# Kernel optimization log

Hardware: AMD Instinct MI355X
Metric: run time of the kernel (lower is better)

## Reference

```python
import jax, jax.numpy as jnp
import numpy as np

N = 100000
E = 1600000
D = 128          # in_feat == hidden_size
L = 3            # hidden layers
EPS = 1e-5       # BatchNorm1d eps


def setup_inputs() -> dict:
    key = jax.random.key(0)
    ks = jax.random.split(key, 12)
    x = jax.random.normal(ks[0], (N, D), dtype=jnp.float32)
    edge_index = jax.random.randint(ks[1], (2, E), 0, N, dtype=jnp.int64)
    s = 1.0 / np.sqrt(D)
    # stacked hidden-layer SAGEConv params: lin_l (neighbor), lin_r (root), bias on lin_l
    Wl = jax.random.uniform(ks[2], (L, D, D), jnp.float32, -s, s)
    Wr = jax.random.uniform(ks[3], (L, D, D), jnp.float32, -s, s)
    b = jax.random.uniform(ks[4], (L, D), jnp.float32, -s, s)
    # batchnorm affine params
    gamma = jnp.ones((L, D), jnp.float32)
    beta = jnp.zeros((L, D), jnp.float32)
    # output SAGEConv: D -> 1
    Wl_out = jax.random.uniform(ks[5], (D, 1), jnp.float32, -s, s)
    Wr_out = jax.random.uniform(ks[6], (D, 1), jnp.float32, -s, s)
    b_out = jax.random.uniform(ks[7], (1,), jnp.float32, -s, s)
    return {"x": x, "edge_index": edge_index, "Wl": Wl, "Wr": Wr, "b": b,
            "gamma": gamma, "beta": beta, "Wl_out": Wl_out, "Wr_out": Wr_out,
            "b_out": b_out}


def _sage(x, src, dst, inv_deg, Wl, Wr, b):
    # gather neighbor features along edges, mean-aggregate at destination
    msg_sum = jax.ops.segment_sum(x[src], dst, num_segments=N)   # [N, F]
    mean = msg_sum * inv_deg                                     # 0 for isolated nodes
    return mean @ Wl + x @ Wr + b


def _batchnorm(x, gamma, beta):
    m = jnp.mean(x, axis=0)
    v = jnp.mean((x - m) ** 2, axis=0)  # biased var, as torch BN uses for normalization
    return gamma * (x - m) * jax.lax.rsqrt(v + EPS) + beta


def reference(x, edge_index, Wl, Wr, b, gamma, beta, Wl_out, Wr_out, b_out):
    src, dst = edge_index[0], edge_index[1]
    deg = jax.ops.segment_sum(jnp.ones((E,), x.dtype), dst, num_segments=N)
    inv_deg = jnp.where(deg > 0, 1.0 / jnp.maximum(deg, 1.0), 0.0)[:, None]
    h = x
    for i in range(L):
        h = _sage(h, src, dst, inv_deg, Wl[i], Wr[i], b[i])
        h = jax.nn.relu(h)
        h = _batchnorm(h, gamma[i], beta[i])
    out = _sage(h, src, dst, inv_deg, Wl_out, Wr_out, b_out)
    return jax.nn.sigmoid(out)  # [N, 1]
```

## Files before the change

kernel.cpp:

```cpp
#include <hip/hip_runtime.h>

typedef unsigned short u16;
typedef unsigned int u32;
typedef unsigned long long u64;

#define GN 100000
#define GE 1600000
#define DCAP 64
#define NRANGE 196
#define NBKT (NRANGE * 8)
#define BCAP 1536

typedef __bf16 bf16x8 __attribute__((ext_vector_type(8)));
typedef float f32x4 __attribute__((ext_vector_type(4)));
typedef float f32x2 __attribute__((ext_vector_type(2)));
typedef u32 u32x4 __attribute__((ext_vector_type(4)));
typedef u32 u32x2 __attribute__((ext_vector_type(2)));

__device__ __forceinline__ float bl(u32 u){ return __uint_as_float(u << 16); }
__device__ __forceinline__ float bh(u32 u){ return __uint_as_float(u & 0xffff0000u); }
__device__ __forceinline__ float bfu(u16 v){ return __uint_as_float(((u32)v) << 16); }
__device__ __forceinline__ u16 f2bf(float f){
    u32 u = __float_as_uint(f);
    u32 r = (u + 0x7fffu + ((u >> 16) & 1u)) >> 16;
    return (u16)r;
}
__device__ __forceinline__ u32 pack2(float a, float b){
    return (u32)f2bf(a) | ((u32)f2bf(b) << 16);
}
__device__ __forceinline__ u32 pk8x4(float a, float b, float c, float d){
    u32 p = (u32)__builtin_amdgcn_cvt_pk_fp8_f32(a, b, 0, false);
    p = (u32)__builtin_amdgcn_cvt_pk_fp8_f32(c, d, p, true);
    return p;
}

__global__ void __launch_bounds__(256) k_init(const int* ei, const u32* xraw,
                                              int* cursor, float* colpart, int* flags,
                                              int* bcur, float* scshbuf){
    int i = blockIdx.x * 256 + threadIdx.x;
    if (i < GN) cursor[i] = 0;
    if (i < NBKT) bcur[i] = 0;
    if (i < 6144) colpart[i] = 0.f;
    if (i < 256) scshbuf[i] = (i < 128) ? 1.f : 0.f;
    int t = threadIdx.x;
    if (blockIdx.x == 0){
        __shared__ int s_any[4];
        int v = 0;
        #pragma unroll
        for (int j = 0; j < 4; ++j){
            int k = t * 4 + j;
            v |= ei[2 * k * 1000 + 1];
        }
        #pragma unroll
        for (int m = 1; m < 64; m <<= 1) v |= __shfl_xor(v, m);
        if ((t & 63) == 0) s_any[t >> 6] = v;
        __syncthreads();
        if (t == 0){
            int any = s_any[0] | s_any[1] | s_any[2] | s_any[3];
            flags[0] = (any == 0) ? 1 : 0;
        }
    }
    if (blockIdx.x == 1){
        __shared__ int s_cnt[4];
        int cnt = 0;
        #pragma unroll
        for (int j = 0; j < 4; ++j){
            int idx = (t * 4 + j) * 6000 + 3;
            u32 u = xraw[idx];
            int e = (u >> 7) & 0xFF;
            cnt += (e >= 100 && e <= 140) ? 1 : 0;
        }
        #pragma unroll
        for (int m = 1; m < 64; m <<= 1) cnt += __shfl_xor(cnt, m);
        if ((t & 63) == 0) s_cnt[t >> 6] = cnt;
        __syncthreads();
        if (t == 0){
            int tot = s_cnt[0] + s_cnt[1] + s_cnt[2] + s_cnt[3];
            flags[1] = (tot > 512) ? 0 : 1;
        }
    }
}

__global__ void __launch_bounds__(256) k_convx(const void* x, const int* flags,
                                               u16* xb, u32* h8){
    int gid = blockIdx.x * 256 + threadIdx.x;
    if (gid >= GN * 16) return;
    float f0,f1,f2,f3,f4,f5,f6,f7;
    if (flags[1]){
        const u32x4* xf = (const u32x4*)x;
        u32x4 a = __builtin_nontemporal_load(xf + gid * 2);
        u32x4 b = __builtin_nontemporal_load(xf + gid * 2 + 1);
        f0 = __uint_as_float(a.x); f1 = __uint_as_float(a.y);
        f2 = __uint_as_float(a.z); f3 = __uint_as_float(a.w);
        f4 = __uint_as_float(b.x); f5 = __uint_as_float(b.y);
        f6 = __uint_as_float(b.z); f7 = __uint_as_float(b.w);
    } else {
        u32x4 g = __builtin_nontemporal_load((const u32x4*)x + gid);
        f0 = bl(g.x); f1 = bh(g.x); f2 = bl(g.y); f3 = bh(g.y);
        f4 = bl(g.z); f5 = bh(g.z); f6 = bl(g.w); f7 = bh(g.w);
    }
    u32x4 o;
    o.x = pack2(f0, f1); o.y = pack2(f2, f3);
    o.z = pack2(f4, f5); o.w = pack2(f6, f7);
    ((u32x4*)xb)[gid] = o;
    u32x2 e = { pk8x4(f0, f1, f2, f3), pk8x4(f4, f5, f6, f7) };
    ((u32x2*)h8)[gid] = e;
}

__global__ void __launch_bounds__(256) k_tofp8(const u16* h, u32* h8){
    int gid = blockIdx.x * 256 + threadIdx.x;
    if (gid >= GN * 16) return;
    u32x4 g = ((const u32x4*)h)[gid];
    u32x2 e = { pk8x4(bl(g.x), bh(g.x), bl(g.y), bh(g.y)),
                pk8x4(bl(g.z), bh(g.z), bl(g.w), bh(g.w)) };
    ((u32x2*)h8)[gid] = e;
}

#define WOFF_WR    49152
#define WOFF_B     98304
#define WOFF_G     98688
#define WOFF_BE    99072
#define WOFF_WLO   99456
#define WOFF_WRO   99584
#define WOFF_BO    99712
#define WTOT       99713
__global__ void __launch_bounds__(256) k_convw(const void* Wl, const void* Wr, const void* b,
                                               const void* g, const void* be, const void* wlo,
                                               const void* wro, const void* bo,
                                               const int* flags, u16* wbuf, float* biasf){
    int i = blockIdx.x * 256 + threadIdx.x;
    if (i >= WTOT) return;
    const void* s; int k;
    if (i < WOFF_B){
        const void* src = (i < WOFF_WR) ? Wl : Wr;
        int r = (i < WOFF_WR) ? i : i - WOFF_WR;
        int layer = r >> 14, L = r & 16383;
        int kk = ((L >> 10) << 3) | (L & 7);
        int cc = (L >> 3) & 127;
        int si = layer * 16384 + kk * 128 + cc;
        float fv = flags[1] ? ((const float*)src)[si] : bfu(((const u16*)src)[si]);
        wbuf[i] = f2bf(fv);
        return;
    }
    if      (i < WOFF_G  ){ s = b;   k = i - WOFF_B; }
    else if (i < WOFF_BE ){ s = g;   k = i - WOFF_G; }
    else if (i < WOFF_WLO){ s = be;  k = i - WOFF_BE; }
    else if (i < WOFF_WRO){ s = wlo; k = i - WOFF_WLO; }
    else if (i < WOFF_BO ){ s = wro; k = i - WOFF_WRO; }
    else                  { s = bo;  k = 0; }
    float fv = flags[1] ? ((const float*)s)[k] : bfu(((const u16*)s)[k]);
    wbuf[i] = f2bf(fv);
    if (i >= WOFF_B && i < WOFF_B + 384) biasf[i - WOFF_B] = fv;
}

__global__ void __launch_bounds__(256) k_fillA(const int* ei, const int* flags,
                                               int* bcur, u64* pairs){
    __shared__ int cnt[256];
    __shared__ int lofs[256];
    __shared__ int gbase[NRANGE];
    __shared__ u64 lp[1024];
    int t = threadIdx.x;
    int res = blockIdx.x & 7;
    int base = blockIdx.x * 1024;
    int is64 = flags[0];
    cnt[t] = 0;
    __syncthreads();
    int myd[4], mys[4], slot[4], myr[4];
    #pragma unroll
    for (int j = 0; j < 4; ++j){
        int e = base + j * 256 + t;
        if (e < GE){
            int d, s;
            if (is64){ d = __builtin_nontemporal_load(ei + 2 * (GE + e));
                       s = __builtin_nontemporal_load(ei + 2 * e); }
            else     { d = __builtin_nontemporal_load(ei + GE + e);
                       s = __builtin_nontemporal_load(ei + e); }
            myd[j] = d; mys[j] = s; myr[j] = d >> 9;
            slot[j] = atomicAdd(&cnt[myr[j]], 1);
        } else myr[j] = -1;
    }
    __syncthreads();
    int v = cnt[t];
    lofs[t] = v; __syncthreads();
    for (int off = 1; off < 256; off <<= 1){
        int u = (t >= off) ? lofs[t - off] : 0;
        __syncthreads();
        lofs[t] += u;
        __syncthreads();
    }
    int incl = lofs[t];
    __syncthreads();
    lofs[t] = incl - v;
    __syncthreads();
    #pragma unroll
    for (int j = 0; j < 4; ++j){
        if (myr[j] >= 0)
            lp[lofs[myr[j]] + slot[j]] = ((u64)(u32)myd[j] << 32) | (u32)mys[j];
    }
    if (t < NRANGE && cnt[t] > 0)
        gbase[t] = atomicAdd(&bcur[t * 8 + res], cnt[t]);
    __syncthreads();
    int total = GE - base; if (total > 1024) total = 1024;
    for (int i = t; i < total; i += 256){
        u64 pr = lp[i];
        int r = (int)(pr >> 32) >> 9;
        int g = gbase[r] + (i - lofs[r]);
        if (g < BCAP) pairs[((size_t)(r * 8 + res)) * BCAP + g] = pr;
    }
}

__global__ void __launch_bounds__(256) k_fillB(const int* bcur, const u64* pairs,
                                               int* cursor, int* col){
    int range = blockIdx.x % 200;
    int sub   = blockIdx.x / 200;
    if (range >= NRANGE || sub >= 8) return;
    int bkt = range * 8 + sub;
    int n = bcur[bkt]; if (n > BCAP) n = BCAP;
    const u64* P = pairs + (size_t)bkt * BCAP;
    for (int i = threadIdx.x; i < n; i += 256){
        u64 pr = __builtin_nontemporal_load(P + i);
        int s = (int)(u32)pr, d = (int)(pr >> 32);
        int pos = atomicAdd(&cursor[d], 1);
        if (pos < DCAP) col[d * DCAP + pos] = s;
    }
}

__global__ void __launch_bounds__(64) k_agg(const u32* h8, const int* deg, const int* col,
                                            u16* amean){
    int lane = threadIdx.x;
    int grp = lane >> 4;
    int lg  = lane & 15;
    int node = blockIdx.x * 4 + grp;
    if (node >= GN) return;
    int d = deg[node];
    int cnt = d < DCAP ? d : DCAP;
    const int* nb = col + node * DCAP;
    const u32x2* hrow = (const u32x2*)h8;
    float a0=0.f,a1=0.f,a2=0.f,a3=0.f,a4=0.f,a5=0.f,a6=0.f,a7=0.f;
    int e = 0;
    #define ACC8(v) { \
        f32x2 d0 = __builtin_amdgcn_cvt_pk_f32_fp8((v).x, false); \
        f32x2 d1 = __builtin_amdgcn_cvt_pk_f32_fp8((v).x, true);  \
        f32x2 d2 = __builtin_amdgcn_cvt_pk_f32_fp8((v).y, false); \
        f32x2 d3 = __builtin_amdgcn_cvt_pk_f32_fp8((v).y, true);  \
        a0 += d0.x; a1 += d0.y; a2 += d1.x; a3 += d1.y;           \
        a4 += d2.x; a5 += d2.y; a6 += d3.x; a7 += d3.y; }
    for (; e + 7 < cnt; e += 8){
        u32x2 v0 = hrow[(size_t)nb[e]     * 16 + lg];
        u32x2 v1 = hrow[(size_t)nb[e + 1] * 16 + lg];
        u32x2 v2 = hrow[(size_t)nb[e + 2] * 16 + lg];
        u32x2 v3 = hrow[(size_t)nb[e + 3] * 16 + lg];
        u32x2 v4 = hrow[(size_t)nb[e + 4] * 16 + lg];
        u32x2 v5 = hrow[(size_t)nb[e + 5] * 16 + lg];
        u32x2 v6 = hrow[(size_t)nb[e + 6] * 16 + lg];
        u32x2 v7 = hrow[(size_t)nb[e + 7] * 16 + lg];
        ACC8(v0) ACC8(v1) ACC8(v2) ACC8(v3) ACC8(v4) ACC8(v5) ACC8(v6) ACC8(v7)
    }
    for (; e + 1 < cnt; e += 2){
        u32x2 v0 = hrow[(size_t)nb[e]     * 16 + lg];
        u32x2 v1 = hrow[(size_t)nb[e + 1] * 16 + lg];
        ACC8(v0) ACC8(v1)
    }
    if (e < cnt){
        u32x2 v0 = hrow[(size_t)nb[e] * 16 + lg];
        ACC8(v0)
    }
    #undef ACC8
    float inv = (d > 0) ? 1.f / (float)d : 0.f;
    u32x4 o;
    o.x = pack2(a0 * inv, a1 * inv);
    o.y = pack2(a2 * inv, a3 * inv);
    o.z = pack2(a4 * inv, a5 * inv);
    o.w = pack2(a6 * inv, a7 * inv);
    ((u32x4*)amean)[(size_t)node * 16 + lg] = o;
}

__global__ void __launch_bounds__(256, 4) k_gemm(const u16* amean, const u16* hin,
                                                 const u16* Wl, const u16* Wr,
                                                 const float* biasf, const float* scsh,
                                                 u16* hout, float* colpart){
    __shared__ __align__(16) u16 wlds[16384];
    int t = threadIdx.x;
    int wid = t >> 6, lane = t & 63;
    int quad = lane >> 4, l15 = lane & 15;
    int r0 = blockIdx.x * 128 + wid * 32;
    int rowa = r0 + l15, rowb = rowa + 16;
    f32x4 acc[2][8];
    #pragma unroll
    for (int i = 0; i < 2; i++)
        #pragma unroll
        for (int j = 0; j < 8; j++) acc[i][j] = (f32x4){0.f, 0.f, 0.f, 0.f};

    #pragma unroll
    for (int half = 0; half < 2; ++half){
        const u16* W = half ? Wr : Wl;
        const u16* A = half ? hin : amean;
        if (half) __syncthreads();
        for (int j = t; j < 2048; j += 256){
            u32x4 g = ((const u32x4*)W)[j];
            int k0 = (j >> 7) << 3;
            f32x4 s0 = *(const f32x4*)(scsh + k0);
            f32x4 s1 = *(const f32x4*)(scsh + k0 + 4);
            u32x4 o;
            o.x = pack2(bl(g.x) * s0.x, bh(g.x) * s0.y);
            o.y = pack2(bl(g.y) * s0.z, bh(g.y) * s0.w);
            o.z = pack2(bl(g.z) * s1.x, bh(g.z) * s1.y);
            o.w = pack2(bl(g.w) * s1.z, bh(g.w) * s1.w);
            ((u32x4*)wlds)[j] = o;
        }
        __syncthreads();
        #pragma unroll
        for (int s = 0; s < 4; ++s){
            int kk = (s << 5) + (quad << 3);
            union { u32x4 u; bf16x8 v; } fa0, fa1;
            fa0.u = (rowa < GN) ? *(const u32x4*)(A + rowa * 128 + kk) : (u32x4){0,0,0,0};
            fa1.u = (rowb < GN) ? *(const u32x4*)(A + rowb * 128 + kk) : (u32x4){0,0,0,0};
            int kc = (s << 2) + quad;
            const u16* wb = &wlds[(kc << 10) + (l15 << 3)];
            #pragma unroll
            for (int cb = 0; cb < 8; ++cb){
                union { u32x4 u; bf16x8 v; } fb;
                fb.u = *(const u32x4*)(wb + (cb << 7));
                acc[0][cb] = __builtin_amdgcn_mfma_f32_16x16x32_bf16(fa0.v, fb.v, acc[0][cb], 0, 0, 0);
                acc[1][cb] = __builtin_amdgcn_mfma_f32_16x16x32_bf16(fa1.v, fb.v, acc[1][cb], 0, 0, 0);
            }
        }
    }
    __syncthreads();
    float* sst = (float*)wlds;
    sst[t] = 0.f;
    __syncthreads();

    float bsv[8];
    #pragma unroll
    for (int cb = 0; cb < 8; cb++) bsv[cb] = biasf[cb * 16 + l15];

    #pragma unroll
    for (int cb = 0; cb < 8; cb++){
        float csum = 0.f, csq = 0.f;
        #pragma unroll
        for (int rb = 0; rb < 2; rb++){
            int rbase = r0 + rb * 16 + quad * 4;
            #pragma unroll
            for (int rr = 0; rr < 4; rr++){
                int row = rbase + rr;
                float v = acc[rb][cb][rr] + bsv[cb];
                v = fmaxf(v, 0.f);
                if (row < GN) hout[row * 128 + cb * 16 + l15] = f2bf(v);
                float vm = (row < GN) ? v : 0.f;
                csum += vm; csq += vm * vm;
            }
        }
        csum += __shfl_xor(csum, 16); csum += __shfl_xor(csum, 32);
        csq  += __shfl_xor(csq, 16);  csq  += __shfl_xor(csq, 32);
        if (quad == 0){
            atomicAdd(&sst[cb * 16 + l15], csum);
            atomicAdd(&sst[128 + cb * 16 + l15], csq);
        }
    }
    __syncthreads();
    atomicAdd(&colpart[(blockIdx.x & 7) * 256 + t], sst[t]);
}

__global__ void __launch_bounds__(256) k_bnf(const float* colpart, const u16* gamma, const u16* beta,
                                             float* scshout, int mode,
                                             const u16* WlN, const u16* WrN,
                                             const float* bNsrc, float* bNdst,
                                             const u16* wlo, const u16* wro, const u16* bo,
                                             u16* hwl, u16* hwr, float* hb){
    __shared__ float s_sc[128], s_sh[128], s_red[256];
    int t = threadIdx.x;
    if (t < 128){
        float s = 0.f, q = 0.f;
        #pragma unroll
        for (int j = 0; j < 8; ++j){
            s += colpart[j * 256 + t];
            q += colpart[j * 256 + 128 + t];
        }
        const float invn = 1.f / (float)GN;
        float mean = s * invn;
        float var = fmaxf(q * invn - mean * mean, 0.f);
        float rstd = rsqrtf(var + 1e-5f);
        float g  = bfu(gamma[t]);
        float be = bfu(beta[t]);
        float sc = g * rstd, sh = be - mean * sc;
        scshout[t] = sc; scshout[128 + t] = sh;
        s_sc[t] = sc; s_sh[t] = sh;
    }
    __syncthreads();
    if (mode == 0){
        if (t < 128){
            float acc = bNsrc[t];
            for (int k = 0; k < 128; ++k){
                int L = ((k >> 3) << 10) + (t << 3) + (k & 7);
                acc += s_sh[k] * (bfu(WlN[L]) + bfu(WrN[L]));
            }
            bNdst[t] = acc;
        }
    } else {
        float contrib = 0.f;
        if (t < 128){
            float wl = bfu(wlo[t]), wr = bfu(wro[t]);
            hwl[t] = f2bf(s_sc[t] * wl);
            hwr[t] = f2bf(s_sc[t] * wr);
            contrib = s_sh[t] * (wl + wr);
        }
        s_red[t] = contrib;
        __syncthreads();
        for (int off = 128; off >= 1; off >>= 1){
            if (t < off) s_red[t] += s_red[t + off];
            __syncthreads();
        }
        if (t == 0) hb[0] = s_red[0] + bfu(bo[0]);
    }
}

__global__ void __launch_bounds__(256) k_dot(const u16* h, const u16* wl, const u16* wr,
                                             float* y, float* r){
    int node = (blockIdx.x * 256 + threadIdx.x) >> 6;
    int lane = threadIdx.x & 63;
    if (node >= GN) return;
    u32 hv  = ((const u32*)h)[node * 64 + lane];
    u32 wlv = ((const u32*)wl)[lane];
    u32 wrv = ((const u32*)wr)[lane];
    float hlo = bl(hv), hhi = bh(hv);
    float ya = hlo * bl(wlv) + hhi * bh(wlv);
    float ra = hlo * bl(wrv) + hhi * bh(wrv);
    #pragma unroll
    for (int m = 1; m < 64; m <<= 1){ ya += __shfl_xor(ya, m); ra += __shfl_xor(ra, m); }
    if (lane == 0){ y[node] = ya; r[node] = ra; }
}

__global__ void __launch_bounds__(256) k_out(const float* y, const float* r, const int* deg,
                                             const int* col, const float* hb,
                                             const int* flags, void* out){
    int n = blockIdx.x * 256 + threadIdx.x;
    if (n >= GN) return;
    int d = deg[n];
    int cnt = d < DCAP ? d : DCAP;
    const int* nb = col + n * DCAP;
    float s = 0.f;
    for (int e = 0; e < cnt; ++e) s += y[nb[e]];
    float inv = (d > 0) ? 1.f / (float)d : 0.f;
    float z = inv * s + r[n] + hb[0];
    float sg = 1.f / (1.f + __expf(-z));
    if (flags[1]) ((float*)out)[n] = sg;
    else          ((u16*)out)[n] = f2bf(sg);
}

extern "C" void kernel_launch(void* const* d_in, const int* in_sizes, int n_in,
                              void* d_out, int out_size, void* d_ws, size_t ws_size,
                              hipStream_t stream) {
    const void* x     = d_in[0];
    const int*  ei    = (const int*)d_in[1];
    const void* Wl    = d_in[2];
    const void* Wr    = d_in[3];
    const void* bias  = d_in[4];
    const void* gamma = d_in[5];
    const void* beta  = d_in[6];
    const void* wlout = d_in[7];
    const void* wrout = d_in[8];
    const void* bout  = d_in[9];

    char* p = (char*)d_ws;
    auto take = [&](size_t b){ void* q = (void*)p; p += (b + 255) & ~(size_t)255; return q; };
    int*   cursor = (int*)  take((size_t)GN * 4);
    int*   flags  = (int*)  take(256);
    int*   bcur   = (int*)  take((size_t)NBKT * 4);
    float* colpart= (float*)take(6144 * 4);
    float* scshbuf= (float*)take(4 * 256 * 4);
    float* biasf  = (float*)take(384 * 4);
    float* bf2    = (float*)take(128 * 4);
    float* bf3    = (float*)take(128 * 4);
    float* hb     = (float*)take(256);
    u16*   hwl    = (u16*)  take(128 * 2);
    u16*   hwr    = (u16*)  take(128 * 2);
    float* yv     = (float*)take((size_t)GN * 4);
    float* rv     = (float*)take((size_t)GN * 4);
    int*   col    = (int*)  take((size_t)GN * DCAP * 4);
    u16*   xb     = (u16*)  take((size_t)GN * 128 * 2);
    u16*   amean  = (u16*)  take((size_t)GN * 128 * 2);
    u16*   hbuf   = (u16*)  take((size_t)GN * 128 * 2);
    u32*   h8     = (u32*)  take((size_t)GN * 128);
    u16*   wbuf   = (u16*)  take((size_t)WTOT * 2);

    u64* pairs = (u64*)amean;

    const int NB_N = (GN + 255) / 256;
    const int NB_A4 = (GN + 3) / 4;
    const int NB_W = (GN + 3) / 4;
    const int NB_G = (GN + 127) / 128;
    const int NB_M = (GN * 16 + 255) / 256;
    const int NB_C = (WTOT + 255) / 256;
    const int NB_A = (GE + 1023) / 1024;

    k_init <<<NB_N, 256, 0, stream>>>(ei, (const u32*)x, cursor, colpart, flags, bcur, scshbuf);
    k_convx<<<NB_M, 256, 0, stream>>>(x, flags, xb, h8);
    k_convw<<<NB_C, 256, 0, stream>>>(Wl, Wr, bias, gamma, beta, wlout, wrout, bout, flags, wbuf, biasf);
    k_fillA<<<NB_A, 256, 0, stream>>>(ei, flags, bcur, pairs);
    k_fillB<<<1600, 256, 0, stream>>>(bcur, pairs, cursor, col);

    const u16* hin = xb;
    for (int i = 0; i < 3; ++i){
        const float* bfi = (i == 0) ? biasf : (i == 1 ? bf2 : bf3);
        float* bNdst = (i == 0) ? bf2 : bf3;
        int nx = (i < 2) ? (i + 1) : 0;
        k_agg <<<NB_A4, 64, 0, stream>>>(h8, cursor, col, amean);
        k_gemm<<<NB_G, 256, 0, stream>>>(amean, hin,
            wbuf + i * 16384, wbuf + WOFF_WR + i * 16384, bfi, scshbuf + i * 256,
            hbuf, colpart + i * 2048);
        k_bnf <<<1,   256, 0, stream>>>(colpart + i * 2048,
            wbuf + WOFF_G + i * 128, wbuf + WOFF_BE + i * 128,
            scshbuf + (i + 1) * 256, (i == 2) ? 1 : 0,
            wbuf + nx * 16384, wbuf + WOFF_WR + nx * 16384, biasf + nx * 128, bNdst,
            wbuf + WOFF_WLO, wbuf + WOFF_WRO, wbuf + WOFF_BO, hwl, hwr, hb);
        if (i < 2) k_tofp8<<<NB_M, 256, 0, stream>>>(hbuf, h8);
        hin = hbuf;
    }
    k_dot<<<NB_W, 256, 0, stream>>>(hbuf, hwl, hwr, yv, rv);
    k_out<<<NB_N, 256, 0, stream>>>(yv, rv, cursor, col, hb, flags, d_out);
}
```

Before: 458.3 us.

## Fuse fp8 conversion into GEMM epilogue via transposed MFMA; use wave-shuffle scan in fillA

The GEMM swaps MFMA operands so each lane holds four consecutive output columns of one node. That lets the epilogue write packed bf16 pairs and emit the fp8 copy of the hidden state directly, which removes the separate k_tofp8 kernel and its extra read of the hidden buffer. The column-statistics reduction now uses a 16-lane shuffle reduction per column group. Separately, the block prefix sum in k_fillA is replaced by a wave-level shuffle scan plus a small cross-wave fix-up, cutting many barriers. The cost is more shuffles in the epilogue and extra fp8 stores inside the GEMM.

```diff
diff --git a/kernel.cpp b/kernel.cpp
--- a/kernel.cpp
+++ b/kernel.cpp
@@ -104,15 +104,6 @@
     o.z = pack2(f4, f5); o.w = pack2(f6, f7);
     ((u32x4*)xb)[gid] = o;
     u32x2 e = { pk8x4(f0, f1, f2, f3), pk8x4(f4, f5, f6, f7) };
-    ((u32x2*)h8)[gid] = e;
-}
-
-__global__ void __launch_bounds__(256) k_tofp8(const u16* h, u32* h8){
-    int gid = blockIdx.x * 256 + threadIdx.x;
-    if (gid >= GN * 16) return;
-    u32x4 g = ((const u32x4*)h)[gid];
-    u32x2 e = { pk8x4(bl(g.x), bh(g.x), bl(g.y), bh(g.y)),
-                pk8x4(bl(g.z), bh(g.z), bl(g.w), bh(g.w)) };
     ((u32x2*)h8)[gid] = e;
 }
 
@@ -158,8 +149,10 @@
     __shared__ int cnt[256];
     __shared__ int lofs[256];
     __shared__ int gbase[NRANGE];
+    __shared__ int wsum[4];
     __shared__ u64 lp[1024];
     int t = threadIdx.x;
+    int lane = t & 63, w = t >> 6;
     int res = blockIdx.x & 7;
     int base = blockIdx.x * 1024;
     int is64 = flags[0];
@@ -181,24 +174,26 @@
     }
     __syncthreads();
     int v = cnt[t];
-    lofs[t] = v; __syncthreads();
-    for (int off = 1; off < 256; off <<= 1){
-        int u = (t >= off) ? lofs[t - off] : 0;
-        __syncthreads();
-        lofs[t] += u;
-        __syncthreads();
-    }
-    int incl = lofs[t];
-    __syncthreads();
-    lofs[t] = incl - v;
+    int sv = v;
+    #pragma unroll
+    for (int d = 1; d < 64; d <<= 1){
+        int u = __shfl_up(sv, d);
+        if (lane >= d) sv += u;
+    }
+    if (lane == 63) wsum[w] = sv;
+    __syncthreads();
+    int prefix = 0;
+    #pragma unroll
+    for (int j = 0; j < 4; ++j) if (j < w) prefix += wsum[j];
+    lofs[t] = sv + prefix - v;
+    if (t < NRANGE && cnt[t] > 0)
+        gbase[t] = atomicAdd(&bcur[t * 8 + res], cnt[t]);
     __syncthreads();
     #pragma unroll
     for (int j = 0; j < 4; ++j){
         if (myr[j] >= 0)
             lp[lofs[myr[j]] + slot[j]] = ((u64)(u32)myd[j] << 32) | (u32)mys[j];
     }
-    if (t < NRANGE && cnt[t] > 0)
-        gbase[t] = atomicAdd(&bcur[t * 8 + res], cnt[t]);
     __syncthreads();
     int total = GE - base; if (total > 1024) total = 1024;
     for (int i = t; i < total; i += 256){
@@ -278,13 +273,13 @@
 __global__ void __launch_bounds__(256, 4) k_gemm(const u16* amean, const u16* hin,
                                                  const u16* Wl, const u16* Wr,
                                                  const float* biasf, const float* scsh,
-                                                 u16* hout, float* colpart){
+                                                 u16* hout, u32* h8, int w8, float* colpart){
     __shared__ __align__(16) u16 wlds[16384];
     int t = threadIdx.x;
     int wid = t >> 6, lane = t & 63;
     int quad = lane >> 4, l15 = lane & 15;
     int r0 = blockIdx.x * 128 + wid * 32;
-    int rowa = r0 + l15, rowb = rowa + 16;
+    int node0 = r0 + l15, node1 = r0 + 16 + l15;
     f32x4 acc[2][8];
     #pragma unroll
     for (int i = 0; i < 2; i++)
@@ -312,17 +307,17 @@
         #pragma unroll
         for (int s = 0; s < 4; ++s){
             int kk = (s << 5) + (quad << 3);
-            union { u32x4 u; bf16x8 v; } fa0, fa1;
-            fa0.u = (rowa < GN) ? *(const u32x4*)(A + rowa * 128 + kk) : (u32x4){0,0,0,0};
-            fa1.u = (rowb < GN) ? *(const u32x4*)(A + rowb * 128 + kk) : (u32x4){0,0,0,0};
+            union { u32x4 u; bf16x8 v; } fn0, fn1;
+            fn0.u = (node0 < GN) ? *(const u32x4*)(A + node0 * 128 + kk) : (u32x4){0,0,0,0};
+            fn1.u = (node1 < GN) ? *(const u32x4*)(A + node1 * 128 + kk) : (u32x4){0,0,0,0};
             int kc = (s << 2) + quad;
             const u16* wb = &wlds[(kc << 10) + (l15 << 3)];
             #pragma unroll
-            for (int cb = 0; cb < 8; ++cb){
-                union { u32x4 u; bf16x8 v; } fb;
-                fb.u = *(const u32x4*)(wb + (cb << 7));
-                acc[0][cb] = __builtin_amdgcn_mfma_f32_16x16x32_bf16(fa0.v, fb.v, acc[0][cb], 0, 0, 0);
-                acc[1][cb] = __builtin_amdgcn_mfma_f32_16x16x32_bf16(fa1.v, fb.v, acc[1][cb], 0, 0, 0);
+            for (int ct = 0; ct < 8; ++ct){
+                union { u32x4 u; bf16x8 v; } fw;
+                fw.u = *(const u32x4*)(wb + (ct << 7));
+                acc[0][ct] = __builtin_amdgcn_mfma_f32_16x16x32_bf16(fw.v, fn0.v, acc[0][ct], 0, 0, 0);
+                acc[1][ct] = __builtin_amdgcn_mfma_f32_16x16x32_bf16(fw.v, fn1.v, acc[1][ct], 0, 0, 0);
             }
         }
     }
@@ -331,31 +326,39 @@
     sst[t] = 0.f;
     __syncthreads();
 
-    float bsv[8];
-    #pragma unroll
-    for (int cb = 0; cb < 8; cb++) bsv[cb] = biasf[cb * 16 + l15];
-
-    #pragma unroll
-    for (int cb = 0; cb < 8; cb++){
-        float csum = 0.f, csq = 0.f;
-        #pragma unroll
-        for (int rb = 0; rb < 2; rb++){
-            int rbase = r0 + rb * 16 + quad * 4;
-            #pragma unroll
-            for (int rr = 0; rr < 4; rr++){
-                int row = rbase + rr;
-                float v = acc[rb][cb][rr] + bsv[cb];
-                v = fmaxf(v, 0.f);
-                if (row < GN) hout[row * 128 + cb * 16 + l15] = f2bf(v);
-                float vm = (row < GN) ? v : 0.f;
-                csum += vm; csq += vm * vm;
-            }
-        }
-        csum += __shfl_xor(csum, 16); csum += __shfl_xor(csum, 32);
-        csq  += __shfl_xor(csq, 16);  csq  += __shfl_xor(csq, 32);
-        if (quad == 0){
-            atomicAdd(&sst[cb * 16 + l15], csum);
-            atomicAdd(&sst[128 + cb * 16 + l15], csq);
+    #pragma unroll
+    for (int ct = 0; ct < 8; ++ct){
+        f32x4 bv = *(const f32x4*)(biasf + ct * 16 + quad * 4);
+        float cs0=0.f,cs1=0.f,cs2=0.f,cs3=0.f,cq0=0.f,cq1=0.f,cq2=0.f,cq3=0.f;
+        #pragma unroll
+        for (int nt = 0; nt < 2; ++nt){
+            int node = nt ? node1 : node0;
+            f32x4 a = acc[nt][ct];
+            float v0 = fmaxf(a.x + bv.x, 0.f);
+            float v1 = fmaxf(a.y + bv.y, 0.f);
+            float v2 = fmaxf(a.z + bv.z, 0.f);
+            float v3 = fmaxf(a.w + bv.w, 0.f);
+            if (node < GN){
+                u32x2 st = { pack2(v0, v1), pack2(v2, v3) };
+                *(u32x2*)(hout + node * 128 + ct * 16 + quad * 4) = st;
+                if (w8) h8[node * 32 + ct * 4 + quad] = pk8x4(v0, v1, v2, v3);
+            } else { v0 = v1 = v2 = v3 = 0.f; }
+            cs0 += v0; cs1 += v1; cs2 += v2; cs3 += v3;
+            cq0 += v0*v0; cq1 += v1*v1; cq2 += v2*v2; cq3 += v3*v3;
+        }
+        #pragma unroll
+        for (int m = 1; m < 16; m <<= 1){
+            cs0 += __shfl_xor(cs0, m); cs1 += __shfl_xor(cs1, m);
+            cs2 += __shfl_xor(cs2, m); cs3 += __shfl_xor(cs3, m);
+            cq0 += __shfl_xor(cq0, m); cq1 += __shfl_xor(cq1, m);
+            cq2 += __shfl_xor(cq2, m); cq3 += __shfl_xor(cq3, m);
+        }
+        if (l15 == 0){
+            int cb = ct * 16 + quad * 4;
+            atomicAdd(&sst[cb + 0], cs0); atomicAdd(&sst[cb + 1], cs1);
+            atomicAdd(&sst[cb + 2], cs2); atomicAdd(&sst[cb + 3], cs3);
+            atomicAdd(&sst[128 + cb + 0], cq0); atomicAdd(&sst[128 + cb + 1], cq1);
+            atomicAdd(&sst[128 + cb + 2], cq2); atomicAdd(&sst[128 + cb + 3], cq3);
         }
     }
     __syncthreads();
@@ -508,13 +511,12 @@
         k_agg <<<NB_A4, 64, 0, stream>>>(h8, cursor, col, amean);
         k_gemm<<<NB_G, 256, 0, stream>>>(amean, hin,
             wbuf + i * 16384, wbuf + WOFF_WR + i * 16384, bfi, scshbuf + i * 256,
-            hbuf, colpart + i * 2048);
+            hbuf, h8, (i < 2) ? 1 : 0, colpart + i * 2048);
         k_bnf <<<1,   256, 0, stream>>>(colpart + i * 2048,
             wbuf + WOFF_G + i * 128, wbuf + WOFF_BE + i * 128,
             scshbuf + (i + 1) * 256, (i == 2) ? 1 : 0,
             wbuf + nx * 16384, wbuf + WOFF_WR + nx * 16384, biasf + nx * 128, bNdst,
             wbuf + WOFF_WLO, wbuf + WOFF_WRO, wbuf + WOFF_BO, hwl, hwr, hb);
-        if (i < 2) k_tofp8<<<NB_M, 256, 0, stream>>>(hbuf, h8);
         hin = hbuf;
     }
     k_dot<<<NB_W, 256, 0, stream>>>(hbuf, hwl, hwr, yv, rv);
```

New measurement: 479.6 us. +4.6%, slower.

## Fuse neighbor aggregation into GEMM and prefold BN scale into next-layer weights

Applied to the files above, without the earlier changes.

Merges the mean-aggregation kernel into the GEMM kernel. Each wave aggregates its 32 rows into an LDS tile, so the bf16 amean array no longer makes a round trip through global memory. The BatchNorm scale is folded into the next layer's weights once, spread over 64 extra blocks of the BN-finalize kernel, and the GEMM reads these prescaled weights directly from global memory instead of rescaling them into LDS in every block. Separately, the scan in the fillA edge-bucketing kernel switches to wave shuffles. The risks are that the gather now shares occupancy with MFMA work in one kernel, and weight fragments now come from global/L2 rather than LDS.

```diff
diff --git a/kernel.cpp b/kernel.cpp
--- a/kernel.cpp
+++ b/kernel.cpp
@@ -36,12 +36,11 @@
 
 __global__ void __launch_bounds__(256) k_init(const int* ei, const u32* xraw,
                                               int* cursor, float* colpart, int* flags,
-                                              int* bcur, float* scshbuf){
+                                              int* bcur){
     int i = blockIdx.x * 256 + threadIdx.x;
     if (i < GN) cursor[i] = 0;
     if (i < NBKT) bcur[i] = 0;
     if (i < 6144) colpart[i] = 0.f;
-    if (i < 256) scshbuf[i] = (i < 128) ? 1.f : 0.f;
     int t = threadIdx.x;
     if (blockIdx.x == 0){
         __shared__ int s_any[4];
@@ -158,8 +157,10 @@
     __shared__ int cnt[256];
     __shared__ int lofs[256];
     __shared__ int gbase[NRANGE];
+    __shared__ int wsum[4];
     __shared__ u64 lp[1024];
     int t = threadIdx.x;
+    int lane = t & 63, w = t >> 6;
     int res = blockIdx.x & 7;
     int base = blockIdx.x * 1024;
     int is64 = flags[0];
@@ -181,24 +182,26 @@
     }
     __syncthreads();
     int v = cnt[t];
-    lofs[t] = v; __syncthreads();
-    for (int off = 1; off < 256; off <<= 1){
-        int u = (t >= off) ? lofs[t - off] : 0;
-        __syncthreads();
-        lofs[t] += u;
-        __syncthreads();
-    }
-    int incl = lofs[t];
-    __syncthreads();
-    lofs[t] = incl - v;
+    int sv = v;
+    #pragma unroll
+    for (int d = 1; d < 64; d <<= 1){
+        int u = __shfl_up(sv, d);
+        if (lane >= d) sv += u;
+    }
+    if (lane == 63) wsum[w] = sv;
+    __syncthreads();
+    int prefix = 0;
+    #pragma unroll
+    for (int j = 0; j < 4; ++j) if (j < w) prefix += wsum[j];
+    lofs[t] = sv + prefix - v;
+    if (t < NRANGE && cnt[t] > 0)
+        gbase[t] = atomicAdd(&bcur[t * 8 + res], cnt[t]);
     __syncthreads();
     #pragma unroll
     for (int j = 0; j < 4; ++j){
         if (myr[j] >= 0)
             lp[lofs[myr[j]] + slot[j]] = ((u64)(u32)myd[j] << 32) | (u32)mys[j];
     }
-    if (t < NRANGE && cnt[t] > 0)
-        gbase[t] = atomicAdd(&bcur[t * 8 + res], cnt[t]);
     __syncthreads();
     int total = GE - base; if (total > 1024) total = 1024;
     for (int i = t; i < total; i += 256){
@@ -225,66 +228,65 @@
     }
 }
 
-__global__ void __launch_bounds__(64) k_agg(const u32* h8, const int* deg, const int* col,
-                                            u16* amean){
-    int lane = threadIdx.x;
-    int grp = lane >> 4;
-    int lg  = lane & 15;
-    int node = blockIdx.x * 4 + grp;
-    if (node >= GN) return;
-    int d = deg[node];
-    int cnt = d < DCAP ? d : DCAP;
-    const int* nb = col + node * DCAP;
-    const u32x2* hrow = (const u32x2*)h8;
-    float a0=0.f,a1=0.f,a2=0.f,a3=0.f,a4=0.f,a5=0.f,a6=0.f,a7=0.f;
-    int e = 0;
-    #define ACC8(v) { \
-        f32x2 d0 = __builtin_amdgcn_cvt_pk_f32_fp8((v).x, false); \
-        f32x2 d1 = __builtin_amdgcn_cvt_pk_f32_fp8((v).x, true);  \
-        f32x2 d2 = __builtin_amdgcn_cvt_pk_f32_fp8((v).y, false); \
-        f32x2 d3 = __builtin_amdgcn_cvt_pk_f32_fp8((v).y, true);  \
-        a0 += d0.x; a1 += d0.y; a2 += d1.x; a3 += d1.y;           \
-        a4 += d2.x; a5 += d2.y; a6 += d3.x; a7 += d3.y; }
-    for (; e + 7 < cnt; e += 8){
-        u32x2 v0 = hrow[(size_t)nb[e]     * 16 + lg];
-        u32x2 v1 = hrow[(size_t)nb[e + 1] * 16 + lg];
-        u32x2 v2 = hrow[(size_t)nb[e + 2] * 16 + lg];
-        u32x2 v3 = hrow[(size_t)nb[e + 3] * 16 + lg];
-        u32x2 v4 = hrow[(size_t)nb[e + 4] * 16 + lg];
-        u32x2 v5 = hrow[(size_t)nb[e + 5] * 16 + lg];
-        u32x2 v6 = hrow[(size_t)nb[e + 6] * 16 + lg];
-        u32x2 v7 = hrow[(size_t)nb[e + 7] * 16 + lg];
-        ACC8(v0) ACC8(v1) ACC8(v2) ACC8(v3) ACC8(v4) ACC8(v5) ACC8(v6) ACC8(v7)
-    }
-    for (; e + 1 < cnt; e += 2){
-        u32x2 v0 = hrow[(size_t)nb[e]     * 16 + lg];
-        u32x2 v1 = hrow[(size_t)nb[e + 1] * 16 + lg];
-        ACC8(v0) ACC8(v1)
-    }
-    if (e < cnt){
-        u32x2 v0 = hrow[(size_t)nb[e] * 16 + lg];
-        ACC8(v0)
-    }
-    #undef ACC8
-    float inv = (d > 0) ? 1.f / (float)d : 0.f;
-    u32x4 o;
-    o.x = pack2(a0 * inv, a1 * inv);
-    o.y = pack2(a2 * inv, a3 * inv);
-    o.z = pack2(a4 * inv, a5 * inv);
-    o.w = pack2(a6 * inv, a7 * inv);
-    ((u32x4*)amean)[(size_t)node * 16 + lg] = o;
-}
-
-__global__ void __launch_bounds__(256, 4) k_gemm(const u16* amean, const u16* hin,
-                                                 const u16* Wl, const u16* Wr,
-                                                 const float* biasf, const float* scsh,
-                                                 u16* hout, float* colpart){
-    __shared__ __align__(16) u16 wlds[16384];
+__global__ void __launch_bounds__(256, 4) k_aggemm(const u32* h8, const int* deg, const int* col,
+                                                   const u16* hin, const u16* Wlp, const u16* Wrp,
+                                                   const float* biasf,
+                                                   u16* hout, float* colpart){
+    __shared__ __align__(16) u16 albuf[4][32][136];
     int t = threadIdx.x;
     int wid = t >> 6, lane = t & 63;
-    int quad = lane >> 4, l15 = lane & 15;
-    int r0 = blockIdx.x * 128 + wid * 32;
-    int rowa = r0 + l15, rowb = rowa + 16;
+    int grp = lane >> 4, lg = lane & 15;
+    int r0w = blockIdx.x * 128 + wid * 32;
+
+    const u32x2* hrow = (const u32x2*)h8;
+    #pragma unroll 1
+    for (int round = 0; round < 8; ++round){
+        int nl = round * 4 + grp;
+        int node = r0w + nl;
+        float a0=0.f,a1=0.f,a2=0.f,a3=0.f,a4=0.f,a5=0.f,a6=0.f,a7=0.f;
+        if (node < GN){
+            int d = deg[node];
+            int cnt = d < DCAP ? d : DCAP;
+            const int* nb = col + node * DCAP;
+            int e = 0;
+            #define ACC8(v) { \
+                f32x2 d0 = __builtin_amdgcn_cvt_pk_f32_fp8((v).x, false); \
+                f32x2 d1 = __builtin_amdgcn_cvt_pk_f32_fp8((v).x, true);  \
+                f32x2 d2 = __builtin_amdgcn_cvt_pk_f32_fp8((v).y, false); \
+                f32x2 d3 = __builtin_amdgcn_cvt_pk_f32_fp8((v).y, true);  \
+                a0 += d0.x; a1 += d0.y; a2 += d1.x; a3 += d1.y;           \
+                a4 += d2.x; a5 += d2.y; a6 += d3.x; a7 += d3.y; }
+            for (; e + 7 < cnt; e += 8){
+                u32x2 v0 = hrow[(size_t)nb[e]     * 16 + lg];
+                u32x2 v1 = hrow[(size_t)nb[e + 1] * 16 + lg];
+                u32x2 v2 = hrow[(size_t)nb[e + 2] * 16 + lg];
+                u32x2 v3 = hrow[(size_t)nb[e + 3] * 16 + lg];
+                u32x2 v4 = hrow[(size_t)nb[e + 4] * 16 + lg];
+                u32x2 v5 = hrow[(size_t)nb[e + 5] * 16 + lg];
+                u32x2 v6 = hrow[(size_t)nb[e + 6] * 16 + lg];
+                u32x2 v7 = hrow[(size_t)nb[e + 7] * 16 + lg];
+                ACC8(v0) ACC8(v1) ACC8(v2) ACC8(v3) ACC8(v4) ACC8(v5) ACC8(v6) ACC8(v7)
+            }
+            for (; e + 1 < cnt; e += 2){
+                u32x2 v0 = hrow[(size_t)nb[e]     * 16 + lg];
+                u32x2 v1 = hrow[(size_t)nb[e + 1] * 16 + lg];
+                ACC8(v0) ACC8(v1)
+            }
+            if (e < cnt){
+                u32x2 v0 = hrow[(size_t)nb[e] * 16 + lg];
+                ACC8(v0)
+            }
+            #undef ACC8
+            float inv = (d > 0) ? 1.f / (float)d : 0.f;
+            a0*=inv; a1*=inv; a2*=inv; a3*=inv; a4*=inv; a5*=inv; a6*=inv; a7*=inv;
+        }
+        u32x4 o;
+        o.x = pack2(a0, a1); o.y = pack2(a2, a3);
+        o.z = pack2(a4, a5); o.w = pack2(a6, a7);
+        *(u32x4*)(&albuf[wid][nl][lg * 8]) = o;
+    }
+
+    int quad = grp, l15 = lg;
     f32x4 acc[2][8];
     #pragma unroll
     for (int i = 0; i < 2; i++)
@@ -293,44 +295,37 @@
 
     #pragma unroll
     for (int half = 0; half < 2; ++half){
-        const u16* W = half ? Wr : Wl;
-        const u16* A = half ? hin : amean;
-        if (half) __syncthreads();
-        for (int j = t; j < 2048; j += 256){
-            u32x4 g = ((const u32x4*)W)[j];
-            int k0 = (j >> 7) << 3;
-            f32x4 s0 = *(const f32x4*)(scsh + k0);
-            f32x4 s1 = *(const f32x4*)(scsh + k0 + 4);
-            u32x4 o;
-            o.x = pack2(bl(g.x) * s0.x, bh(g.x) * s0.y);
-            o.y = pack2(bl(g.y) * s0.z, bh(g.y) * s0.w);
-            o.z = pack2(bl(g.z) * s1.x, bh(g.z) * s1.y);
-            o.w = pack2(bl(g.w) * s1.z, bh(g.w) * s1.w);
-            ((u32x4*)wlds)[j] = o;
-        }
-        __syncthreads();
+        const u16* W = half ? Wrp : Wlp;
         #pragma unroll
         for (int s = 0; s < 4; ++s){
             int kk = (s << 5) + (quad << 3);
-            union { u32x4 u; bf16x8 v; } fa0, fa1;
-            fa0.u = (rowa < GN) ? *(const u32x4*)(A + rowa * 128 + kk) : (u32x4){0,0,0,0};
-            fa1.u = (rowb < GN) ? *(const u32x4*)(A + rowb * 128 + kk) : (u32x4){0,0,0,0};
+            union { u32x4 u; bf16x8 v; } fn0, fn1;
+            if (half == 0){
+                fn0.u = *(const u32x4*)(&albuf[wid][l15][kk]);
+                fn1.u = *(const u32x4*)(&albuf[wid][l15 + 16][kk]);
+            } else {
+                int n0 = r0w + l15, n1 = r0w + 16 + l15;
+                fn0.u = (n0 < GN) ? *(const u32x4*)(hin + n0 * 128 + kk) : (u32x4){0,0,0,0};
+                fn1.u = (n1 < GN) ? *(const u32x4*)(hin + n1 * 128 + kk) : (u32x4){0,0,0,0};
+            }
             int kc = (s << 2) + quad;
-            const u16* wb = &wlds[(kc << 10) + (l15 << 3)];
+            const u32x4* wg = (const u32x4*)W + (kc << 7) + l15;
             #pragma unroll
             for (int cb = 0; cb < 8; ++cb){
-                union { u32x4 u; bf16x8 v; } fb;
-                fb.u = *(const u32x4*)(wb + (cb << 7));
-                acc[0][cb] = __builtin_amdgcn_mfma_f32_16x16x32_bf16(fa0.v, fb.v, acc[0][cb], 0, 0, 0);
-                acc[1][cb] = __builtin_amdgcn_mfma_f32_16x16x32_bf16(fa1.v, fb.v, acc[1][cb], 0, 0, 0);
-            }
-        }
-    }
-    __syncthreads();
-    float* sst = (float*)wlds;
+                union { u32x4 u; bf16x8 v; } fw;
+                fw.u = wg[cb << 4];
+                acc[0][cb] = __builtin_amdgcn_mfma_f32_16x16x32_bf16(fn0.v, fw.v, acc[0][cb], 0, 0, 0);
+                acc[1][cb] = __builtin_amdgcn_mfma_f32_16x16x32_bf16(fn1.v, fw.v, acc[1][cb], 0, 0, 0);
+            }
+        }
+    }
+
+    __syncthreads();
+    float* sst = (float*)albuf;
     sst[t] = 0.f;
     __syncthreads();
 
+    int r0 = r0w;
     float bsv[8];
     #pragma unroll
     for (int cb = 0; cb < 8; cb++) bsv[cb] = biasf[cb * 16 + l15];
@@ -363,13 +358,13 @@
 }
 
 __global__ void __launch_bounds__(256) k_bnf(const float* colpart, const u16* gamma, const u16* beta,
-                                             float* scshout, int mode,
-                                             const u16* WlN, const u16* WrN,
+                                             int mode,
+                                             const u16* WlN, const u16* WrN, u16* wfd,
                                              const float* bNsrc, float* bNdst,
                                              const u16* wlo, const u16* wro, const u16* bo,
                                              u16* hwl, u16* hwr, float* hb){
     __shared__ float s_sc[128], s_sh[128], s_red[256];
-    int t = threadIdx.x;
+    int t = threadIdx.x, b = blockIdx.x;
     if (t < 128){
         float s = 0.f, q = 0.f;
         #pragma unroll
@@ -384,12 +379,17 @@
         float g  = bfu(gamma[t]);
         float be = bfu(beta[t]);
         float sc = g * rstd, sh = be - mean * sc;
-        scshout[t] = sc; scshout[128 + t] = sh;
         s_sc[t] = sc; s_sh[t] = sh;
     }
     __syncthreads();
     if (mode == 0){
-        if (t < 128){
+        if (b < 64){
+            int idx = b * 256 + t;
+            int k = ((idx >> 10) << 3) | (idx & 7);
+            float sc = s_sc[k];
+            wfd[idx]         = f2bf(sc * bfu(WlN[idx]));
+            wfd[16384 + idx] = f2bf(sc * bfu(WrN[idx]));
+        } else if (t < 128){
             float acc = bNsrc[t];
             for (int k = 0; k < 128; ++k){
                 int L = ((k >> 3) << 10) + (t << 3) + (k & 7);
@@ -397,7 +397,7 @@
             }
             bNdst[t] = acc;
         }
-    } else {
+    } else if (b == 64){
         float contrib = 0.f;
         if (t < 128){
             float wl = bfu(wlo[t]), wr = bfu(wro[t]);
@@ -468,33 +468,33 @@
     int*   flags  = (int*)  take(256);
     int*   bcur   = (int*)  take((size_t)NBKT * 4);
     float* colpart= (float*)take(6144 * 4);
-    float* scshbuf= (float*)take(4 * 256 * 4);
     float* biasf  = (float*)take(384 * 4);
     float* bf2    = (float*)take(128 * 4);
     float* bf3    = (float*)take(128 * 4);
     float* hb     = (float*)take(256);
+    u16*   wf2    = (u16*)  take(32768 * 2);
+    u16*   wf3    = (u16*)  take(32768 * 2);
     u16*   hwl    = (u16*)  take(128 * 2);
     u16*   hwr    = (u16*)  take(128 * 2);
     float* yv     = (float*)take((size_t)GN * 4);
     float* rv     = (float*)take((size_t)GN * 4);
     int*   col    = (int*)  take((size_t)GN * DCAP * 4);
     u16*   xb     = (u16*)  take((size_t)GN * 128 * 2);
-    u16*   amean  = (u16*)  take((size_t)GN * 128 * 2);
+    u16*   scrap  = (u16*)  take((size_t)GN * 128 * 2);
     u16*   hbuf   = (u16*)  take((size_t)GN * 128 * 2);
     u32*   h8     = (u32*)  take((size_t)GN * 128);
     u16*   wbuf   = (u16*)  take((size_t)WTOT * 2);
 
-    u64* pairs = (u64*)amean;
+    u64* pairs = (u64*)scrap;
 
     const int NB_N = (GN + 255) / 256;
-    const int NB_A4 = (GN + 3) / 4;
     const int NB_W = (GN + 3) / 4;
     const int NB_G = (GN + 127) / 128;
     const int NB_M = (GN * 16 + 255) / 256;
     const int NB_C = (WTOT + 255) / 256;
     const int NB_A = (GE + 1023) / 1024;
 
-    k_init <<<NB_N, 256, 0, stream>>>(ei, (const u32*)x, cursor, colpart, flags, bcur, scshbuf);
+    k_init <<<NB_N, 256, 0, stream>>>(ei, (const u32*)x, cursor, colpart, flags, bcur);
     k_convx<<<NB_M, 256, 0, stream>>>(x, flags, xb, h8);
     k_convw<<<NB_C, 256, 0, stream>>>(Wl, Wr, bias, gamma, beta, wlout, wrout, bout, flags, wbuf, biasf);
     k_fillA<<<NB_A, 256, 0, stream>>>(ei, flags, bcur, pairs);
@@ -502,17 +502,19 @@
 
     const u16* hin = xb;
     for (int i = 0; i < 3; ++i){
-        const float* bfi = (i == 0) ? biasf : (i == 1 ? bf2 : bf3);
+        const u16* Wlp; const u16* Wrp; const float* bfi;
+        if (i == 0){ Wlp = wbuf;     Wrp = wbuf + WOFF_WR; bfi = biasf; }
+        else if (i == 1){ Wlp = wf2; Wrp = wf2 + 16384;    bfi = bf2; }
+        else { Wlp = wf3;            Wrp = wf3 + 16384;    bfi = bf3; }
+        u16* wfd = (i == 0) ? wf2 : wf3;
         float* bNdst = (i == 0) ? bf2 : bf3;
         int nx = (i < 2) ? (i + 1) : 0;
-        k_agg <<<NB_A4, 64, 0, stream>>>(h8, cursor, col, amean);
-        k_gemm<<<NB_G, 256, 0, stream>>>(amean, hin,
-            wbuf + i * 16384, wbuf + WOFF_WR + i * 16384, bfi, scshbuf + i * 256,
-            hbuf, colpart + i * 2048);
-        k_bnf <<<1,   256, 0, stream>>>(colpart + i * 2048,
-            wbuf + WOFF_G + i * 128, wbuf + WOFF_BE + i * 128,
-            scshbuf + (i + 1) * 256, (i == 2) ? 1 : 0,
-            wbuf + nx * 16384, wbuf + WOFF_WR + nx * 16384, biasf + nx * 128, bNdst,
+        k_aggemm<<<NB_G, 256, 0, stream>>>(h8, cursor, col, hin, Wlp, Wrp, bfi, hbuf,
+                                           colpart + i * 2048);
+        k_bnf  <<<65, 256, 0, stream>>>(colpart + i * 2048,
+            wbuf + WOFF_G + i * 128, wbuf + WOFF_BE + i * 128, (i == 2) ? 1 : 0,
+            wbuf + nx * 16384, wbuf + WOFF_WR + nx * 16384, wfd,
+            biasf + nx * 128, bNdst,
             wbuf + WOFF_WLO, wbuf + WOFF_WRO, wbuf + WOFF_BO, hwl, hwr, hb);
         if (i < 2) k_tofp8<<<NB_M, 256, 0, stream>>>(hbuf, h8);
         hin = hbuf;
```

Measured after the change: 457.5 us. About the same (-0.2%).
